# Performance work log

Measured on AMD Instinct MI355X. Metric: run time of the kernel, lower is better.

The kernel has to match this reference:

```python
import jax, jax.numpy as jnp
import numpy as np

N = 100_000          # nodes
E = 3_200_000        # train edges (avg degree 32)
E_TEST = 500_000     # pos/neg test edges each
F_IN, F_HID, F_OUT = 256, 16, 64


def setup_inputs() -> dict:
    key = jax.random.key(0)
    ks = jax.random.split(key, 7)
    x = jax.random.normal(ks[0], (N, F_IN), jnp.float32)
    train_edge_index = jax.random.randint(ks[1], (2, E), 0, N, dtype=jnp.int32)
    test_pos_edge_index = jax.random.randint(ks[2], (2, E_TEST), 0, N, dtype=jnp.int32)
    test_neg_edge_index = jax.random.randint(ks[3], (2, E_TEST), 0, N, dtype=jnp.int32)
    W1 = jax.random.normal(ks[4], (F_IN, F_HID), jnp.float32) / np.float32(np.sqrt(F_IN))
    b1 = jnp.zeros((F_HID,), jnp.float32)
    W2 = jax.random.normal(ks[5], (F_HID, F_OUT), jnp.float32) / np.float32(np.sqrt(F_HID))
    b2 = jnp.zeros((F_OUT,), jnp.float32)
    return dict(x=x, train_edge_index=train_edge_index,
                test_pos_edge_index=test_pos_edge_index,
                test_neg_edge_index=test_neg_edge_index,
                W1=W1, b1=b1, W2=W2, b2=b2)


def gcn_conv(x, edge_index, W, b, n):
    """PyG GCNConv: x' = D^-1/2 (A+I) D^-1/2 (x W) + b (self-loops added)."""
    h = x @ W                                  # project first (PyG order)
    loop = jnp.arange(n, dtype=edge_index.dtype)
    src = jnp.concatenate([edge_index[0], loop])
    dst = jnp.concatenate([edge_index[1], loop])
    deg = jax.ops.segment_sum(jnp.ones_like(dst, dtype=h.dtype), dst, num_segments=n)
    dinv = jnp.where(deg > 0, jax.lax.rsqrt(deg), 0.0)
    norm = dinv[src] * dinv[dst]               # per-edge symmetric norm
    msg = h[src] * norm[:, None]               # gather + scale
    out = jax.ops.segment_sum(msg, dst, num_segments=n)  # scatter-add
    return out + b


def reference(x, train_edge_index, test_pos_edge_index, test_neg_edge_index,
              W1, b1, W2, b2):
    n = x.shape[0]
    z = gcn_conv(x, train_edge_index, W1, b1, n)
    z = jax.nn.relu(z)
    z = gcn_conv(z, train_edge_index, W2, b2, n)
    edge_index = jnp.concatenate([test_pos_edge_index, test_neg_edge_index], axis=-1)
    logits = jnp.sum(z[edge_index[0]] * z[edge_index[1]], axis=-1)
    return logits
```

## Files before the change

### kernel.cpp

```cpp
#include <hip/hip_runtime.h>


#define CAP   18432
#define CHUNK 4096

__global__ void seedprep_kernel(int* __restrict__ gtail, int nb1,
                                const float* __restrict__ W2, const float* __restrict__ b2,
                                float* __restrict__ mw) {
    int t = threadIdx.x;
    if (t < nb1) gtail[t] = t * CAP;
    int r = t >> 4, cc = t & 15;
    float s = 0.0f;
    for (int j = 0; j < 64; ++j) s += W2[r * 64 + j] * W2[cc * 64 + j];
    mw[t] = s;
    if (t < 16) {
        float w = 0.0f;
        for (int j = 0; j < 64; ++j) w += W2[t * 64 + j] * b2[j];
        mw[256 + t] = w;
    }
    if (t == 0) {
        float bbv = 0.0f;
        for (int j = 0; j < 64; ++j) bbv += b2[j] * b2[j];
        mw[272] = bbv;
    }
}

__global__ void passA1_kernel(const int* __restrict__ src, const int* __restrict__ dst, int E,
                              int* __restrict__ gtail, unsigned* __restrict__ tmp, int nb1) {
    __shared__ int cnt[256];
    __shared__ int base[256];
    int t = threadIdx.x;
    int c0 = blockIdx.x * CHUNK;
    if (t < nb1) cnt[t] = 0;
    __syncthreads();
    unsigned rec[16];
    unsigned brk[16];
    #pragma unroll
    for (int j = 0; j < 16; ++j) {
        int e = c0 + t + j * 256;
        if (e < E) {
            int s = src[e], d = dst[e];
            int b = d >> 9;
            int r = atomicAdd(&cnt[b], 1);
            rec[j] = (unsigned)s | ((unsigned)(d & 511) << 20);
            brk[j] = ((unsigned)b << 16) | (unsigned)r;
        }
    }
    __syncthreads();
    if (t < nb1) base[t] = atomicAdd(&gtail[t], cnt[t]);
    __syncthreads();
    #pragma unroll
    for (int j = 0; j < 16; ++j) {
        int e = c0 + t + j * 256;
        if (e < E) {
            int b = (int)(brk[j] >> 16), r = (int)(brk[j] & 0xFFFFu);
            tmp[base[b] + r] = rec[j];
        }
    }
}

__global__ void fill2_kernel(const int* __restrict__ gtail, const unsigned* __restrict__ tmp,
                             int* __restrict__ eidx, int* __restrict__ rowptr,
                             int* __restrict__ counts, float* __restrict__ dinv, int n) {
    int b = blockIdx.x;
    int t = threadIdx.x;
    int beg = b * CAP;
    int cnt_total = gtail[b] - beg;
    __shared__ int h[512];
    __shared__ int cur[512];
    h[t] = 0; h[t + 256] = 0;
    __syncthreads();
    for (int i = t; i < cnt_total; i += 256) {
        unsigned r = tmp[beg + i];
        atomicAdd(&h[r >> 20], 1);
    }
    __syncthreads();
    if (t == 0) {
        int run = beg;
        for (int j = 0; j < 512; ++j) { int c = h[j]; cur[j] = run; run += c; }
    }
    __syncthreads();
    for (int j = t; j < 512; j += 256) {
        int v = (b << 9) + j;
        if (v < n) {
            rowptr[v] = cur[j];
            counts[v] = h[j];
            dinv[v]   = rsqrtf((float)h[j] + 1.0f);
        }
    }
    __syncthreads();
    for (int i = t; i < cnt_total; i += 256) {
        unsigned r = tmp[beg + i];
        int p = atomicAdd(&cur[r >> 20], 1);
        eidx[p] = (int)(r & 0xFFFFF);
    }
}

__global__ void __launch_bounds__(64)
gemm1_kernel(const float* __restrict__ x, const float* __restrict__ W1,
             const float* __restrict__ dinv, float* __restrict__ hs, int n) {
    int row = blockIdx.x * 64 + threadIdx.x;
    if (row >= n) return;
    const float4* x4 = (const float4*)(x + (size_t)row * 256);
    const float4* W14 = (const float4*)W1;
    float4 a0 = {0,0,0,0}, a1 = {0,0,0,0}, a2 = {0,0,0,0}, a3 = {0,0,0,0};
    float4 buf[8];
    #pragma unroll
    for (int j = 0; j < 8; ++j) buf[j] = x4[j];
    for (int k8 = 0; k8 < 8; ++k8) {
        float4 cur[8];
        #pragma unroll
        for (int j = 0; j < 8; ++j) cur[j] = buf[j];
        if (k8 < 7) {
            #pragma unroll
            for (int j = 0; j < 8; ++j) buf[j] = x4[(k8 + 1) * 8 + j];
        }
        #pragma unroll
        for (int jj = 0; jj < 8; ++jj) {
            float4 xv = cur[jj];
            int k4 = k8 * 8 + jj;
            #pragma unroll
            for (int j = 0; j < 4; ++j) {
                float xk = (j == 0) ? xv.x : (j == 1) ? xv.y : (j == 2) ? xv.z : xv.w;
                int k = (k4 << 2) + j;
                float4 w0 = W14[k * 4 + 0];
                float4 w1 = W14[k * 4 + 1];
                float4 w2 = W14[k * 4 + 2];
                float4 w3 = W14[k * 4 + 3];
                a0.x += xk * w0.x; a0.y += xk * w0.y; a0.z += xk * w0.z; a0.w += xk * w0.w;
                a1.x += xk * w1.x; a1.y += xk * w1.y; a1.z += xk * w1.z; a1.w += xk * w1.w;
                a2.x += xk * w2.x; a2.y += xk * w2.y; a2.z += xk * w2.z; a2.w += xk * w2.w;
                a3.x += xk * w3.x; a3.y += xk * w3.y; a3.z += xk * w3.z; a3.w += xk * w3.w;
            }
        }
    }
    float di = dinv[row];
    float4* o = (float4*)(hs + (size_t)row * 16);
    a0.x *= di; a0.y *= di; a0.z *= di; a0.w *= di;
    a1.x *= di; a1.y *= di; a1.z *= di; a1.w *= di;
    a2.x *= di; a2.y *= di; a2.z *= di; a2.w *= di;
    a3.x *= di; a3.y *= di; a3.z *= di; a3.w *= di;
    o[0] = a0; o[1] = a1; o[2] = a2; o[3] = a3;
}

__global__ void agg1_kernel(const int* __restrict__ rowptr, const int* __restrict__ counts,
                            const int* __restrict__ eidx, const float4* __restrict__ hs4,
                            const float* __restrict__ dinv, const float* __restrict__ b1,
                            float4* __restrict__ gs4, int n) {
    int t = blockIdx.x * blockDim.x + threadIdx.x;
    int v = t >> 3;
    if (v >= n) return;
    int q = t & 3, hh = (t >> 2) & 1;
    int start = rowptr[v], cnt = counts[v];
    float4 s = {0, 0, 0, 0};
    int i = hh;
    for (; i + 6 < cnt; i += 8) {
        int s0 = eidx[start + i];
        int s1 = eidx[start + i + 2];
        int s2 = eidx[start + i + 4];
        int s3 = eidx[start + i + 6];
        float4 h0 = hs4[(size_t)s0 * 4 + q];
        float4 h1 = hs4[(size_t)s1 * 4 + q];
        float4 h2 = hs4[(size_t)s2 * 4 + q];
        float4 h3 = hs4[(size_t)s3 * 4 + q];
        s.x += h0.x + h1.x + h2.x + h3.x;
        s.y += h0.y + h1.y + h2.y + h3.y;
        s.z += h0.z + h1.z + h2.z + h3.z;
        s.w += h0.w + h1.w + h2.w + h3.w;
    }
    for (; i < cnt; i += 2) {
        float4 h0 = hs4[(size_t)eidx[start + i] * 4 + q];
        s.x += h0.x; s.y += h0.y; s.z += h0.z; s.w += h0.w;
    }
    s.x += __shfl_xor(s.x, 4);
    s.y += __shfl_xor(s.y, 4);
    s.z += __shfl_xor(s.z, 4);
    s.w += __shfl_xor(s.w, 4);
    if (hh == 0) {
        float di = dinv[v];
        float4 h = hs4[(size_t)v * 4 + q];
        float4 b = ((const float4*)b1)[q];
        float4 z;
        z.x = fmaxf(di * (s.x + h.x) + b.x, 0.0f) * di;
        z.y = fmaxf(di * (s.y + h.y) + b.y, 0.0f) * di;
        z.z = fmaxf(di * (s.z + h.z) + b.z, 0.0f) * di;
        z.w = fmaxf(di * (s.w + h.w) + b.w, 0.0f) * di;
        gs4[(size_t)v * 4 + q] = z;
    }
}

__global__ void agg2y_kernel(const int* __restrict__ rowptr, const int* __restrict__ counts,
                             const int* __restrict__ eidx, const float4* __restrict__ gs4,
                             const float* __restrict__ dinv, const float* __restrict__ mw,
                             float4* __restrict__ u4, float* __restrict__ y,
                             float* __restrict__ c, int n) {
    __shared__ float su[32 * 16];
    __shared__ float sM[256];
    __shared__ float sw[16];
    int t = threadIdx.x;
    sM[t] = mw[t];
    if (t < 16) sw[t] = mw[256 + t];

    int j = t >> 3, q = t & 3, hh = (t >> 2) & 1;
    int v = blockIdx.x * 32 + j;
    if (v < n) {
        int start = rowptr[v], cnt = counts[v];
        float4 s = {0, 0, 0, 0};
        int i = hh;
        for (; i + 6 < cnt; i += 8) {
            int s0 = eidx[start + i];
            int s1 = eidx[start + i + 2];
            int s2 = eidx[start + i + 4];
            int s3 = eidx[start + i + 6];
            float4 g0 = gs4[(size_t)s0 * 4 + q];
            float4 g1 = gs4[(size_t)s1 * 4 + q];
            float4 g2 = gs4[(size_t)s2 * 4 + q];
            float4 g3 = gs4[(size_t)s3 * 4 + q];
            s.x += g0.x + g1.x + g2.x + g3.x;
            s.y += g0.y + g1.y + g2.y + g3.y;
            s.z += g0.z + g1.z + g2.z + g3.z;
            s.w += g0.w + g1.w + g2.w + g3.w;
        }
        for (; i < cnt; i += 2) {
            float4 g0 = gs4[(size_t)eidx[start + i] * 4 + q];
            s.x += g0.x; s.y += g0.y; s.z += g0.z; s.w += g0.w;
        }
        s.x += __shfl_xor(s.x, 4);
        s.y += __shfl_xor(s.y, 4);
        s.z += __shfl_xor(s.z, 4);
        s.w += __shfl_xor(s.w, 4);
        if (hh == 0) {
            float di = dinv[v];
            float4 g = gs4[(size_t)v * 4 + q];
            float4 uu;
            uu.x = di * (s.x + g.x);
            uu.y = di * (s.y + g.y);
            uu.z = di * (s.z + g.z);
            uu.w = di * (s.w + g.w);
            float* up = &su[j * 16 + q * 4];
            up[0] = uu.x; up[1] = uu.y; up[2] = uu.z; up[3] = uu.w;
            u4[(size_t)v * 4 + q] = uu;
        }
    }
    __syncthreads();
    if (v < n) {
        int l8 = t & 7;
        const float* uu = &su[j * 16];
        int c0 = l8 * 2;
        float y0 = sw[c0], y1 = sw[c0 + 1];
        #pragma unroll
        for (int k = 0; k < 16; ++k) {
            float uk = uu[k];
            y0 += uk * sM[k * 16 + c0];
            y1 += uk * sM[k * 16 + c0 + 1];
        }
        float2* yp = (float2*)(y + (size_t)v * 16 + c0);
        *yp = make_float2(y0, y1);
        if (l8 == 0) {
            float cv = 0.0f;
            #pragma unroll
            for (int k = 0; k < 16; ++k) cv += uu[k] * sw[k];
            c[v] = cv;
        }
    }
}

__global__ void edge_dot_kernel(const int* __restrict__ pa, const int* __restrict__ pb,
                                const int* __restrict__ na, const int* __restrict__ nb_,
                                int ET, const float* __restrict__ u, const float* __restrict__ y,
                                const float* __restrict__ c, const float* __restrict__ mw,
                                float* __restrict__ out) {
    int t = blockIdx.x * blockDim.x + threadIdx.x;
    int p = t >> 4, l = t & 15;
    if (p >= ET) return;
    int a0 = pa[p], b0 = pb[p];
    int a1 = na[p], b1 = nb_[p];
    float ya0 = y[(size_t)a0 * 16 + l];
    float ub0 = u[(size_t)b0 * 16 + l];
    float ya1 = y[(size_t)a1 * 16 + l];
    float ub1 = u[(size_t)b1 * 16 + l];
    float p0 = ya0 * ub0;
    float p1 = ya1 * ub1;
    p0 += __shfl_xor(p0, 1);  p1 += __shfl_xor(p1, 1);
    p0 += __shfl_xor(p0, 2);  p1 += __shfl_xor(p1, 2);
    p0 += __shfl_xor(p0, 4);  p1 += __shfl_xor(p1, 4);
    p0 += __shfl_xor(p0, 8);  p1 += __shfl_xor(p1, 8);
    if (l == 0) {
        float bb = mw[272];
        out[p]      = p0 + c[a0] + bb;
        out[ET + p] = p1 + c[a1] + bb;
    }
}

extern "C" void kernel_launch(void* const* d_in, const int* in_sizes, int n_in,
                              void* d_out, int out_size, void* d_ws, size_t ws_size,
                              hipStream_t stream) {
    const float* x    = (const float*)d_in[0];
    const int*   tei  = (const int*)d_in[1];
    const int*   tpos = (const int*)d_in[2];
    const int*   tneg = (const int*)d_in[3];
    const float* W1   = (const float*)d_in[4];
    const float* b1   = (const float*)d_in[5];
    const float* W2   = (const float*)d_in[6];
    const float* b2   = (const float*)d_in[7];
    float* out = (float*)d_out;

    int n   = in_sizes[0] / 256;
    int E   = in_sizes[1] / 2;
    int ET  = in_sizes[2] / 2;
    int nb1 = (n + 511) >> 9;

    char* w = (char*)d_ws;
    int*   gtail  = (int*)w;        w += 256 * 4;
    float* mw     = (float*)w;      w += 512 * 4;
    int*   rowptr = (int*)w;        w += (size_t)n * 4;
    int*   counts = (int*)w;        w += (size_t)n * 4;
    float* dinv   = (float*)w;      w += (size_t)n * 4;
    float* hs     = (float*)w;      w += (size_t)16 * n * 4;
    float* gs     = (float*)w;      w += (size_t)16 * n * 4;
    float* u      = (float*)w;      w += (size_t)16 * n * 4;
    float* y      = (float*)w;      w += (size_t)16 * n * 4;
    float* c      = (float*)w;      w += (size_t)n * 4;
    int*   eidx   = (int*)w;        w += (size_t)nb1 * CAP * 4;
    unsigned* tmp = (unsigned*)w;   w += (size_t)nb1 * CAP * 4;

    const int* src = tei;
    const int* dst = tei + E;

    seedprep_kernel<<<1, 256, 0, stream>>>(gtail, nb1, W2, b2, mw);
    passA1_kernel<<<(E + CHUNK - 1) / CHUNK, 256, 0, stream>>>(src, dst, E, gtail, tmp, nb1);
    fill2_kernel<<<nb1, 256, 0, stream>>>(gtail, tmp, eidx, rowptr, counts, dinv, n);

    gemm1_kernel<<<(n + 63) / 64, 64, 0, stream>>>(x, W1, dinv, hs, n);
    agg1_kernel<<<(8 * n + 255) / 256, 256, 0, stream>>>(rowptr, counts, eidx,
                                                         (const float4*)hs, dinv, b1,
                                                         (float4*)gs, n);
    agg2y_kernel<<<(n + 31) / 32, 256, 0, stream>>>(rowptr, counts, eidx,
                                                    (const float4*)gs, dinv, mw,
                                                    (float4*)u, y, c, n);
    edge_dot_kernel<<<(16 * ET + 255) / 256, 256, 0, stream>>>(tpos, tpos + ET, tneg, tneg + ET,
                                                               ET, u, y, c, mw, out);
}
```

Baseline: 386.2 us.

## Stage bucket scatter in LDS and use finer 256-node buckets for CSR build

The partition pass now histograms each chunk, prefix-scans, and reorders records in shared memory so global writes to each bucket are contiguous runs instead of scattered stores. Buckets shrink to 256 destination nodes (twice as many blocks for the fill pass), and the fill pass stages its output in LDS and writes eidx coalesced. Both kernels use 512 threads and larger chunks. In exchange, LDS usage per block rises, which may limit occupancy, and the capacity per bucket is tighter, which could overflow if degrees are skewed.

```diff
diff --git a/kernel.cpp b/kernel.cpp
--- a/kernel.cpp
+++ b/kernel.cpp
@@ -1,14 +1,15 @@
 #include <hip/hip_runtime.h>
 
 
-#define CAP   18432
-#define CHUNK 4096
+#define NB_SHIFT 8
+#define CAP   9728
+#define CHUNK 8192
 
 __global__ void seedprep_kernel(int* __restrict__ gtail, int nb1,
                                 const float* __restrict__ W2, const float* __restrict__ b2,
                                 float* __restrict__ mw) {
     int t = threadIdx.x;
-    if (t < nb1) gtail[t] = t * CAP;
+    for (int i = t; i < nb1; i += 256) gtail[i] = i * CAP;
     int r = t >> 4, cc = t & 15;
     float s = 0.0f;
     for (int j = 0; j < 64; ++j) s += W2[r * 64 + j] * W2[cc * 64 + j];
@@ -25,75 +26,100 @@
     }
 }
 
-__global__ void passA1_kernel(const int* __restrict__ src, const int* __restrict__ dst, int E,
-                              int* __restrict__ gtail, unsigned* __restrict__ tmp, int nb1) {
-    __shared__ int cnt[256];
-    __shared__ int base[256];
+__global__ void __launch_bounds__(512)
+passA1_kernel(const int* __restrict__ src, const int* __restrict__ dst, int E,
+              int* __restrict__ gtail, unsigned* __restrict__ tmp, int nb1) {
+    __shared__ int h[512];
+    __shared__ int loff[512];
+    __shared__ int cur[512];
+    __shared__ int base[512];
+    __shared__ unsigned srec[CHUNK];
+    __shared__ unsigned short sbkt[CHUNK];
     int t = threadIdx.x;
     int c0 = blockIdx.x * CHUNK;
-    if (t < nb1) cnt[t] = 0;
-    __syncthreads();
-    unsigned rec[16];
-    unsigned brk[16];
-    #pragma unroll
-    for (int j = 0; j < 16; ++j) {
-        int e = c0 + t + j * 256;
-        if (e < E) {
-            int s = src[e], d = dst[e];
-            int b = d >> 9;
-            int r = atomicAdd(&cnt[b], 1);
-            rec[j] = (unsigned)s | ((unsigned)(d & 511) << 20);
-            brk[j] = ((unsigned)b << 16) | (unsigned)r;
-        }
-    }
-    __syncthreads();
-    if (t < nb1) base[t] = atomicAdd(&gtail[t], cnt[t]);
-    __syncthreads();
-    #pragma unroll
-    for (int j = 0; j < 16; ++j) {
-        int e = c0 + t + j * 256;
-        if (e < E) {
-            int b = (int)(brk[j] >> 16), r = (int)(brk[j] & 0xFFFFu);
-            tmp[base[b] + r] = rec[j];
-        }
-    }
-}
-
-__global__ void fill2_kernel(const int* __restrict__ gtail, const unsigned* __restrict__ tmp,
-                             int* __restrict__ eidx, int* __restrict__ rowptr,
-                             int* __restrict__ counts, float* __restrict__ dinv, int n) {
+    int ce = min(CHUNK, E - c0);
+
+    h[t] = 0;
+    __syncthreads();
+    for (int i = t; i < ce; i += 512)
+        atomicAdd(&h[dst[c0 + i] >> NB_SHIFT], 1);
+    __syncthreads();
+    int cnt = h[t];
+    loff[t] = cnt;
+    __syncthreads();
+    for (int off = 1; off < 512; off <<= 1) {
+        int v = loff[t];
+        int a = (t >= off) ? loff[t - off] : 0;
+        __syncthreads();
+        loff[t] = v + a;
+        __syncthreads();
+    }
+    int excl = loff[t] - cnt;
+    if (t < nb1) base[t] = atomicAdd(&gtail[t], cnt);
+    loff[t] = excl;
+    cur[t]  = excl;
+    __syncthreads();
+    for (int i = t; i < ce; i += 512) {
+        int d = dst[c0 + i];
+        int s = src[c0 + i];
+        int b = d >> NB_SHIFT;
+        int p = atomicAdd(&cur[b], 1);
+        srec[p] = (unsigned)s | ((unsigned)(d & 255) << 20);
+        sbkt[p] = (unsigned short)b;
+    }
+    __syncthreads();
+    for (int i = t; i < ce; i += 512) {
+        int b = sbkt[i];
+        tmp[base[b] + (i - loff[b])] = srec[i];
+    }
+}
+
+__global__ void __launch_bounds__(512)
+fill2_kernel(const int* __restrict__ gtail, const unsigned* __restrict__ tmp,
+             int* __restrict__ eidx, int* __restrict__ rowptr,
+             int* __restrict__ counts, float* __restrict__ dinv, int n) {
+    __shared__ int hh[256];
+    __shared__ int sc[256];
+    __shared__ int cur[256];
+    __shared__ int sout[CAP];
     int b = blockIdx.x;
     int t = threadIdx.x;
     int beg = b * CAP;
     int cnt_total = gtail[b] - beg;
-    __shared__ int h[512];
-    __shared__ int cur[512];
-    h[t] = 0; h[t + 256] = 0;
-    __syncthreads();
-    for (int i = t; i < cnt_total; i += 256) {
-        unsigned r = tmp[beg + i];
-        atomicAdd(&h[r >> 20], 1);
-    }
-    __syncthreads();
-    if (t == 0) {
-        int run = beg;
-        for (int j = 0; j < 512; ++j) { int c = h[j]; cur[j] = run; run += c; }
-    }
-    __syncthreads();
-    for (int j = t; j < 512; j += 256) {
-        int v = (b << 9) + j;
+
+    if (t < 256) hh[t] = 0;
+    __syncthreads();
+    for (int i = t; i < cnt_total; i += 512)
+        atomicAdd(&hh[tmp[beg + i] >> 20], 1);
+    __syncthreads();
+    if (t < 256) sc[t] = hh[t];
+    __syncthreads();
+    for (int off = 1; off < 256; off <<= 1) {
+        int v = 0, a = 0;
+        if (t < 256) { v = sc[t]; a = (t >= off) ? sc[t - off] : 0; }
+        __syncthreads();
+        if (t < 256) sc[t] = v + a;
+        __syncthreads();
+    }
+    if (t < 256) {
+        int ex = sc[t] - hh[t];
+        cur[t] = ex;
+        int v = (b << NB_SHIFT) + t;
         if (v < n) {
-            rowptr[v] = cur[j];
-            counts[v] = h[j];
-            dinv[v]   = rsqrtf((float)h[j] + 1.0f);
-        }
-    }
-    __syncthreads();
-    for (int i = t; i < cnt_total; i += 256) {
+            rowptr[v] = beg + ex;
+            counts[v] = hh[t];
+            dinv[v]   = rsqrtf((float)hh[t] + 1.0f);
+        }
+    }
+    __syncthreads();
+    for (int i = t; i < cnt_total; i += 512) {
         unsigned r = tmp[beg + i];
         int p = atomicAdd(&cur[r >> 20], 1);
-        eidx[p] = (int)(r & 0xFFFFF);
-    }
+        sout[p] = (int)(r & 0xFFFFF);
+    }
+    __syncthreads();
+    for (int i = t; i < cnt_total; i += 512)
+        eidx[beg + i] = sout[i];
 }
 
 __global__ void __launch_bounds__(64)
@@ -308,10 +334,10 @@
     int n   = in_sizes[0] / 256;
     int E   = in_sizes[1] / 2;
     int ET  = in_sizes[2] / 2;
-    int nb1 = (n + 511) >> 9;
+    int nb1 = (n + 255) >> NB_SHIFT;
 
     char* w = (char*)d_ws;
-    int*   gtail  = (int*)w;        w += 256 * 4;
+    int*   gtail  = (int*)w;        w += 512 * 4;
     float* mw     = (float*)w;      w += 512 * 4;
     int*   rowptr = (int*)w;        w += (size_t)n * 4;
     int*   counts = (int*)w;        w += (size_t)n * 4;
@@ -328,8 +354,8 @@
     const int* dst = tei + E;
 
     seedprep_kernel<<<1, 256, 0, stream>>>(gtail, nb1, W2, b2, mw);
-    passA1_kernel<<<(E + CHUNK - 1) / CHUNK, 256, 0, stream>>>(src, dst, E, gtail, tmp, nb1);
-    fill2_kernel<<<nb1, 256, 0, stream>>>(gtail, tmp, eidx, rowptr, counts, dinv, n);
+    passA1_kernel<<<(E + CHUNK - 1) / CHUNK, 512, 0, stream>>>(src, dst, E, gtail, tmp, nb1);
+    fill2_kernel<<<nb1, 512, 0, stream>>>(gtail, tmp, eidx, rowptr, counts, dinv, n);
 
     gemm1_kernel<<<(n + 63) / 64, 64, 0, stream>>>(x, W1, dinv, hs, n);
     agg1_kernel<<<(8 * n + 255) / 256, 256, 0, stream>>>(rowptr, counts, eidx,
```

New measurement: 349.6 us. 1.1x faster.
